# Kernel tuning notes

Measured on AMD Instinct MI355X. Metric: run time of the kernel, lower is better.

## Reference

```python
import jax, jax.numpy as jnp
import numpy as np


def setup_inputs() -> dict:
    key = jax.random.key(0)
    k1, k2, k3, k4 = jax.random.split(key, 4)
    B, S, D, H = 64, 512, 1024, 1024
    scale = 1.0 / np.sqrt(H)
    x = jax.random.normal(k1, (B, S, D), dtype=jnp.float32)
    Wx = jax.random.normal(k2, (D, H), dtype=jnp.float32) * scale
    Wh = jax.random.normal(k3, (H, H), dtype=jnp.float32) * scale
    b = jax.random.normal(k4, (H,), dtype=jnp.float32) * scale
    return {"x": x, "Wx": Wx, "Wh": Wh, "b": b}


def reference(x, Wx, Wh, b):
    # Elman tanh RNN cell: h_t = tanh(x_t @ Wx + h_{t-1} @ Wh + b)
    # Truncated BPTT: carried state is detached each step (stop_gradient),
    # matching `state = state.detach()` in the torch forward.
    B, S, D = x.shape
    H = Wh.shape[0]
    h0 = jnp.zeros((B, H), dtype=x.dtype)  # get_initial_state
    # precompute input projections for all timesteps: [S, B, H]
    xw = jnp.swapaxes(jnp.einsum('bsd,dh->bsh', x, Wx) + b, 0, 1)

    def step(h_prev, xw_t):
        h_new = jnp.tanh(xw_t + h_prev @ Wh)
        return jax.lax.stop_gradient(h_new), h_new

    _, hs = jax.lax.scan(step, h0, xw)  # hs: [S, B, H]
    return jnp.swapaxes(hs, 0, 1)  # [B, S, H]
```

## Files before the change

### kernel.cpp

```cpp
#include <hip/hip_runtime.h>
#include <stdint.h>

#define B_  64
#define S_  512
#define D_  1024
#define H_  1024

#define NBLK2 128

typedef __attribute__((ext_vector_type(2))) float    f32x2;
typedef __attribute__((ext_vector_type(4))) float    f32x4;
typedef __attribute__((ext_vector_type(4))) uint32_t u32x4;
typedef __attribute__((ext_vector_type(8))) __bf16   bf16x8;

__device__ __forceinline__ f32x4 mfma16(bf16x8 a, bf16x8 b, f32x4 c) {
  return __builtin_amdgcn_mfma_f32_16x16x32_bf16(a, b, c, 0, 0, 0);
}

__device__ __forceinline__ void gload_lds16(const void* g, void* l) {
  __builtin_amdgcn_global_load_lds(
      (const __attribute__((address_space(1))) void*)g,
      (__attribute__((address_space(3))) void*)l, 16, 0, 0);
}

__device__ __forceinline__ void st_dword_sc(uint32_t* p, uint32_t v) {
  asm volatile("global_store_dword %0, %1, off sc0 sc1" :: "v"(p), "v"(v) : "memory");
}
__device__ __forceinline__ void st_short_sc(uint16_t* p, uint32_t v) {
  asm volatile("global_store_short %0, %1, off sc0 sc1" :: "v"(p), "v"(v) : "memory");
}
__device__ __forceinline__ uint32_t ld_dword_sc(const uint32_t* p) {
  uint32_t r;
  asm volatile("global_load_dword %0, %1, off sc0 sc1\n\t"
               "s_waitcnt vmcnt(0)" : "=v"(r) : "v"(p) : "memory");
  return r;
}
__device__ __forceinline__ void ld_dwordx4_sc_issue(u32x4& dst, const void* p) {
  asm volatile("global_load_dwordx4 %0, %1, off sc0 sc1" : "=v"(dst) : "v"(p));
}

__device__ __forceinline__ uint32_t permhi(uint32_t a, uint32_t b) {
  return __builtin_amdgcn_perm(a, b, 0x07060302u);
}

__device__ __forceinline__ float tanh_fast(float x) {
  float ax = fabsf(x);
  float e = __expf(-2.0f * ax);
  float r = (1.0f - e) / (1.0f + e);
  return x < 0.0f ? -r : r;
}

__device__ __forceinline__ void split8(f32x4 a0, f32x4 a1, bf16x8& hi, bf16x8& lo) {
  float f[8] = {a0.x, a0.y, a0.z, a0.w, a1.x, a1.y, a1.z, a1.w};
  uint32_t hb[8], lb[8];
#pragma unroll
  for (int i = 0; i < 8; ++i) {
    uint32_t b = __builtin_bit_cast(uint32_t, f[i]);
    hb[i] = b;
    float hf = __builtin_bit_cast(float, b & 0xffff0000u);
    lb[i] = __builtin_bit_cast(uint32_t, f[i] - hf);
  }
  u32x4 hv = {permhi(hb[1], hb[0]), permhi(hb[3], hb[2]),
              permhi(hb[5], hb[4]), permhi(hb[7], hb[6])};
  u32x4 lv = {permhi(lb[1], lb[0]), permhi(lb[3], lb[2]),
              permhi(lb[5], lb[4]), permhi(lb[7], lb[6])};
  hi = __builtin_bit_cast(bf16x8, hv);
  lo = __builtin_bit_cast(bf16x8, lv);
}

__global__ __launch_bounds__(256) void prep_kernel(
    const float* __restrict__ Wx, const float* __restrict__ Wh,
    uint16_t* __restrict__ wxt_hi, uint16_t* __restrict__ wxt_lo,
    uint16_t* __restrict__ wht_hi, uint16_t* __restrict__ wht_lo,
    unsigned* __restrict__ flags)
{
  if (blockIdx.x == 0) {
    for (int i = threadIdx.x; i < 1024; i += 256)
      st_dword_sc((uint32_t*)flags + i, 0u);
  }
  __shared__ float tile[32][33];
  int bid = blockIdx.x;
  int mat = bid >> 10;
  int t   = bid & 1023;
  int tk = t >> 5, tn = t & 31;
  const float* src = mat ? Wh : Wx;
  uint16_t* dhi = mat ? wht_hi : wxt_hi;
  uint16_t* dlo = mat ? wht_lo : wxt_lo;
  int tx = threadIdx.x & 31, ty0 = threadIdx.x >> 5;
  int k0 = tk * 32, n0 = tn * 32;
#pragma unroll
  for (int i = 0; i < 4; ++i) {
    int ty = ty0 + 8 * i;
    tile[ty][tx] = src[(size_t)(k0 + ty) * 1024 + n0 + tx];
  }
  __syncthreads();
#pragma unroll
  for (int i = 0; i < 4; ++i) {
    int ty = ty0 + 8 * i;
    float v = tile[tx][ty];
    uint32_t bv = __builtin_bit_cast(uint32_t, v);
    float lo = v - __builtin_bit_cast(float, bv & 0xffff0000u);
    uint32_t lbv = __builtin_bit_cast(uint32_t, lo);
    size_t o = (size_t)(n0 + ty) * 1024 + k0 + tx;
    dhi[o] = (uint16_t)(bv >> 16);
    dlo[o] = (uint16_t)(lbv >> 16);
  }
}

__global__ __launch_bounds__(256) void xw_gemm_kernel(
    const float* __restrict__ x, const uint16_t* __restrict__ wxt_hi,
    const uint16_t* __restrict__ wxt_lo, const float* __restrict__ bias,
    float* __restrict__ out)
{
  __shared__ __align__(16) float    ldsA[128 * 32];
  __shared__ __align__(16) uint16_t ldsBh[128 * 32];
  __shared__ __align__(16) uint16_t ldsBl[128 * 32];

  int bid = blockIdx.x;
  int swz = (bid & 7) * 256 + (bid >> 3);
  int mt = swz >> 3, nt = swz & 7;
  int M0 = mt * 128, N0 = nt * 128;

  int tid = threadIdx.x;
  int w = tid >> 6, l = tid & 63;
  int wm = w >> 1, wn = w & 1;

  int a_row = l >> 3;
  int a_sw  = ((l & 7) ^ (l >> 3)) << 4;
  int b_row = l >> 2;
  int b_sw  = (((l & 3) ^ ((l >> 2) & 3)) << 4);

  f32x4 acc[4][4];
#pragma unroll
  for (int i = 0; i < 4; ++i)
#pragma unroll
    for (int j = 0; j < 4; ++j) acc[i][j] = (f32x4){0.f, 0.f, 0.f, 0.f};

  const char* xb  = (const char*)x;
  const char* bhp = (const char*)wxt_hi;
  const char* blp = (const char*)wxt_lo;

  for (int s = 0; s < 32; ++s) {
#pragma unroll
    for (int j = 0; j < 4; ++j) {
      int i = 4 * w + j;
      const char* g = xb + ((size_t)(M0 + 8 * i + a_row) * 4096) + s * 128 + a_sw;
      gload_lds16(g, (char*)ldsA + i * 1024);
    }
#pragma unroll
    for (int j = 0; j < 2; ++j) {
      int i = 2 * w + j;
      size_t ro = (size_t)(N0 + 16 * i + b_row) * 2048 + s * 64 + b_sw;
      gload_lds16(bhp + ro, (char*)ldsBh + i * 1024);
      gload_lds16(blp + ro, (char*)ldsBl + i * 1024);
    }
    __syncthreads();

    bf16x8 ah[4], al[4], bh[4], bl[4];
#pragma unroll
    for (int mi = 0; mi < 4; ++mi) {
      int row = 64 * wm + 16 * mi + (l & 15);
      int kb  = (l >> 4) * 32;
      int sw  = (row & 7) << 4;
      f32x4 a0 = *(const f32x4*)((const char*)ldsA + row * 128 + (kb ^ sw));
      f32x4 a1 = *(const f32x4*)((const char*)ldsA + row * 128 + ((kb + 16) ^ sw));
      split8(a0, a1, ah[mi], al[mi]);
    }
#pragma unroll
    for (int ni = 0; ni < 4; ++ni) {
      int n  = 64 * wn + 16 * ni + (l & 15);
      int kb = (l >> 4) * 16;
      int off = n * 64 + (kb ^ ((n & 3) << 4));
      bh[ni] = *(const bf16x8*)((const char*)ldsBh + off);
      bl[ni] = *(const bf16x8*)((const char*)ldsBl + off);
    }
#pragma unroll
    for (int mi = 0; mi < 4; ++mi)
#pragma unroll
      for (int ni = 0; ni < 4; ++ni) {
        acc[mi][ni] = mfma16(ah[mi], bh[ni], acc[mi][ni]);
        acc[mi][ni] = mfma16(al[mi], bh[ni], acc[mi][ni]);
        acc[mi][ni] = mfma16(ah[mi], bl[ni], acc[mi][ni]);
      }
    __syncthreads();
  }

#pragma unroll
  for (int ni = 0; ni < 4; ++ni) {
    int col = N0 + 64 * wn + 16 * ni + (l & 15);
    float bv = bias[col];
#pragma unroll
    for (int mi = 0; mi < 4; ++mi) {
      int row0 = M0 + 64 * wm + 16 * mi + 4 * (l >> 4);
#pragma unroll
      for (int r = 0; r < 4; ++r)
        out[(size_t)(row0 + r) * 1024 + col] = acc[mi][ni][r] + bv;
    }
  }
}

__global__ __launch_bounds__(512, 1) void rnn_seq_kernel(
    float* __restrict__ out,
    const uint16_t* wht_hi, const uint16_t* wht_lo,
    uint16_t* __restrict__ hq,
    unsigned* __restrict__ flags)
{
  __shared__ __align__(16) float red[2][8][16][33];

  const int bid = blockIdx.x;
  const int g   = bid >> 5;
  const int c   = bid & 31;
  const int c0  = c * 32;

  const int tid = threadIdx.x;
  const int kw  = tid >> 6;
  const int l   = tid & 63;
  const int lr  = l & 15, lq = l >> 4;

  u32x4 wbh[2][4], wbl[2][4];
#pragma unroll
  for (int n2 = 0; n2 < 2; ++n2) {
    const size_t colb = (size_t)(c0 + n2 * 16 + lr) * 1024 + kw * 128 + lq * 8;
#pragma unroll
    for (int kc = 0; kc < 4; ++kc) {
      wbh[n2][kc] = *(const u32x4*)(wht_hi + colb + kc * 32);
      wbl[n2][kc] = *(const u32x4*)(wht_lo + colb + kc * 32);
    }
  }

  const uint16_t* hb_base = hq + (size_t)(g * 16 + lr) * 1024 + kw * 128 + lq * 8;
  const int HQ = 64 * 1024;

  const int frow = tid >> 5;
  const int fcol = tid & 31;
  const size_t out_base = ((size_t)(g * 16 + frow) * 512) * 1024 + c0 + fcol;
  const size_t h_off    = (size_t)(g * 16 + frow) * 1024 + c0 + fcol;

  const uint32_t* fpoll = (const uint32_t*)flags + g * 256 + kw * 32 + (l & 31);
  uint32_t*       fown  = (uint32_t*)flags + g * 256 + c * 8 + kw;

  for (int t = 0; t < 512; ++t) {
#pragma unroll
    for (int n2 = 0; n2 < 2; ++n2)
#pragma unroll
      for (int kc = 0; kc < 4; ++kc) {
        asm volatile("" : "+v"(wbh[n2][kc]));
        asm volatile("" : "+v"(wbl[n2][kc]));
      }

    float xwv = out[out_base + (size_t)t * 1024];

    f32x4 cH0 = {0.f,0.f,0.f,0.f}, cL0 = {0.f,0.f,0.f,0.f};
    f32x4 cH1 = {0.f,0.f,0.f,0.f}, cL1 = {0.f,0.f,0.f,0.f};

    if (t > 0) {
      const unsigned tgt = (unsigned)t;
      while (true) {
        unsigned v = ld_dword_sc(fpoll);
        if (!__any((int)(v < tgt))) break;
        __builtin_amdgcn_s_sleep(1);
      }
      const uint16_t* hb = hb_base + ((t - 1) & 1) * HQ;
      u32x4 av[4];
#pragma unroll
      for (int kc = 0; kc < 4; ++kc)
        ld_dwordx4_sc_issue(av[kc], hb + kc * 32);
      __builtin_amdgcn_sched_barrier(0);
      asm volatile("s_waitcnt vmcnt(0)" ::: "memory");
      __builtin_amdgcn_sched_barrier(0);
#pragma unroll
      for (int kc = 0; kc < 4; ++kc) {
        bf16x8 a   = __builtin_bit_cast(bf16x8, av[kc]);
        cH0 = mfma16(a, __builtin_bit_cast(bf16x8, wbh[0][kc]), cH0);
        cH1 = mfma16(a, __builtin_bit_cast(bf16x8, wbh[1][kc]), cH1);
        cL0 = mfma16(a, __builtin_bit_cast(bf16x8, wbl[0][kc]), cL0);
        cL1 = mfma16(a, __builtin_bit_cast(bf16x8, wbl[1][kc]), cL1);
      }
    }

    f32x4 acc0 = cH0 + cL0;
    f32x4 acc1 = cH1 + cL1;

    const int rbuf = t & 1;
#pragma unroll
    for (int r = 0; r < 4; ++r) {
      red[rbuf][kw][lq * 4 + r][lr]      = acc0[r];
      red[rbuf][kw][lq * 4 + r][16 + lr] = acc1[r];
    }
    __syncthreads();

    float s = 0.f;
#pragma unroll
    for (int wv = 0; wv < 8; ++wv)
      s += red[rbuf][wv][frow][fcol];

    float hval = tanh_fast(s + xwv);
    out[out_base + (size_t)t * 1024] = hval;

    if (t < 511) {
      uint32_t b  = __builtin_bit_cast(uint32_t, hval);
      uint32_t rb = (b + 0x7fffu + ((b >> 16) & 1u)) >> 16;
      st_short_sc(hq + (size_t)(t & 1) * HQ + h_off, rb);
      asm volatile("s_waitcnt vmcnt(0)" ::: "memory");
      if (l == 0) st_dword_sc(fown, (uint32_t)(t + 1));
    }
  }
}

extern "C" void kernel_launch(void* const* d_in, const int* in_sizes, int n_in,
                              void* d_out, int out_size, void* d_ws, size_t ws_size,
                              hipStream_t stream) {
  const float* x    = (const float*)d_in[0];
  const float* Wx   = (const float*)d_in[1];
  const float* Wh   = (const float*)d_in[2];
  const float* bias = (const float*)d_in[3];
  float* out = (float*)d_out;

  char* ws = (char*)d_ws;
  uint16_t* wxt_hi = (uint16_t*)(ws);
  uint16_t* wxt_lo = (uint16_t*)(ws + (2u << 20));
  uint16_t* wht_hi = (uint16_t*)(ws + (4u << 20));
  uint16_t* wht_lo = (uint16_t*)(ws + (6u << 20));
  uint16_t* hq     = (uint16_t*)(ws + (8u << 20));
  unsigned* flags  = (unsigned*)(ws + (8u << 20) + (1u << 18));

  prep_kernel<<<dim3(2048), dim3(256), 0, stream>>>(Wx, Wh, wxt_hi, wxt_lo,
                                                    wht_hi, wht_lo, flags);
  xw_gemm_kernel<<<dim3(2048), dim3(256), 0, stream>>>(x, wxt_hi, wxt_lo, bias, out);
  rnn_seq_kernel<<<dim3(NBLK2), dim3(512), 0, stream>>>(out, wht_hi, wht_lo,
                                                        hq, flags);
}
```

Baseline: 1.730 ms.

## Replace flag polling with step-tagged hidden-state words for inter-block sync

```diff
diff --git a/kernel.cpp b/kernel.cpp
--- a/kernel.cpp
+++ b/kernel.cpp
@@ -25,15 +25,6 @@
 
 __device__ __forceinline__ void st_dword_sc(uint32_t* p, uint32_t v) {
   asm volatile("global_store_dword %0, %1, off sc0 sc1" :: "v"(p), "v"(v) : "memory");
-}
-__device__ __forceinline__ void st_short_sc(uint16_t* p, uint32_t v) {
-  asm volatile("global_store_short %0, %1, off sc0 sc1" :: "v"(p), "v"(v) : "memory");
-}
-__device__ __forceinline__ uint32_t ld_dword_sc(const uint32_t* p) {
-  uint32_t r;
-  asm volatile("global_load_dword %0, %1, off sc0 sc1\n\t"
-               "s_waitcnt vmcnt(0)" : "=v"(r) : "v"(p) : "memory");
-  return r;
 }
 __device__ __forceinline__ void ld_dwordx4_sc_issue(u32x4& dst, const void* p) {
   asm volatile("global_load_dwordx4 %0, %1, off sc0 sc1" : "=v"(dst) : "v"(p));
@@ -72,11 +63,11 @@
     const float* __restrict__ Wx, const float* __restrict__ Wh,
     uint16_t* __restrict__ wxt_hi, uint16_t* __restrict__ wxt_lo,
     uint16_t* __restrict__ wht_hi, uint16_t* __restrict__ wht_lo,
-    unsigned* __restrict__ flags)
+    uint32_t* __restrict__ hq)
 {
-  if (blockIdx.x == 0) {
-    for (int i = threadIdx.x; i < 1024; i += 256)
-      st_dword_sc((uint32_t*)flags + i, 0u);
+  {
+    int gid = blockIdx.x * 256 + threadIdx.x;
+    if (gid < 2 * 64 * 1024) hq[gid] = 0xFFFFFFFFu;
   }
   __shared__ float tile[32][33];
   int bid = blockIdx.x;
@@ -202,8 +193,7 @@
 __global__ __launch_bounds__(512, 1) void rnn_seq_kernel(
     float* __restrict__ out,
     const uint16_t* wht_hi, const uint16_t* wht_lo,
-    uint16_t* __restrict__ hq,
-    unsigned* __restrict__ flags)
+    uint32_t* __restrict__ hq)
 {
   __shared__ __align__(16) float red[2][8][16][33];
 
@@ -228,7 +218,7 @@
     }
   }
 
-  const uint16_t* hb_base = hq + (size_t)(g * 16 + lr) * 1024 + kw * 128 + lq * 8;
+  const uint32_t* hq_base = hq + (size_t)(g * 16 + lr) * 1024 + kw * 128 + lq * 8;
   const int HQ = 64 * 1024;
 
   const int frow = tid >> 5;
@@ -236,9 +226,6 @@
   const size_t out_base = ((size_t)(g * 16 + frow) * 512) * 1024 + c0 + fcol;
   const size_t h_off    = (size_t)(g * 16 + frow) * 1024 + c0 + fcol;
 
-  const uint32_t* fpoll = (const uint32_t*)flags + g * 256 + kw * 32 + (l & 31);
-  uint32_t*       fown  = (uint32_t*)flags + g * 256 + c * 8 + kw;
-
   for (int t = 0; t < 512; ++t) {
 #pragma unroll
     for (int n2 = 0; n2 < 2; ++n2)
@@ -254,23 +241,38 @@
     f32x4 cH1 = {0.f,0.f,0.f,0.f}, cL1 = {0.f,0.f,0.f,0.f};
 
     if (t > 0) {
-      const unsigned tgt = (unsigned)t;
+      const uint32_t* hb = hq_base + ((t - 1) & 1) * HQ;
+      const uint32_t expect = (uint32_t)(t - 1) & 0xffffu;
+      u32x4 pk[4][2];
       while (true) {
-        unsigned v = ld_dword_sc(fpoll);
-        if (!__any((int)(v < tgt))) break;
+#pragma unroll
+        for (int kc = 0; kc < 4; ++kc) {
+          ld_dwordx4_sc_issue(pk[kc][0], hb + kc * 32);
+          ld_dwordx4_sc_issue(pk[kc][1], hb + kc * 32 + 4);
+        }
+        __builtin_amdgcn_sched_barrier(0);
+        asm volatile("s_waitcnt vmcnt(0)" ::: "memory");
+        __builtin_amdgcn_sched_barrier(0);
+        uint32_t bad = 0;
+#pragma unroll
+        for (int kc = 0; kc < 4; ++kc)
+#pragma unroll
+          for (int j = 0; j < 2; ++j)
+#pragma unroll
+            for (int e = 0; e < 4; ++e)
+              bad |= (pk[kc][j][e] ^ expect);
+        bad &= 0xffffu;
+        if (!__any((int)bad)) break;
         __builtin_amdgcn_s_sleep(1);
       }
-      const uint16_t* hb = hb_base + ((t - 1) & 1) * HQ;
-      u32x4 av[4];
-#pragma unroll
-      for (int kc = 0; kc < 4; ++kc)
-        ld_dwordx4_sc_issue(av[kc], hb + kc * 32);
-      __builtin_amdgcn_sched_barrier(0);
-      asm volatile("s_waitcnt vmcnt(0)" ::: "memory");
-      __builtin_amdgcn_sched_barrier(0);
 #pragma unroll
       for (int kc = 0; kc < 4; ++kc) {
-        bf16x8 a   = __builtin_bit_cast(bf16x8, av[kc]);
+        u32x4 aw;
+        aw[0] = permhi(pk[kc][0][1], pk[kc][0][0]);
+        aw[1] = permhi(pk[kc][0][3], pk[kc][0][2]);
+        aw[2] = permhi(pk[kc][1][1], pk[kc][1][0]);
+        aw[3] = permhi(pk[kc][1][3], pk[kc][1][2]);
+        bf16x8 a = __builtin_bit_cast(bf16x8, aw);
         cH0 = mfma16(a, __builtin_bit_cast(bf16x8, wbh[0][kc]), cH0);
         cH1 = mfma16(a, __builtin_bit_cast(bf16x8, wbh[1][kc]), cH1);
         cL0 = mfma16(a, __builtin_bit_cast(bf16x8, wbl[0][kc]), cL0);
@@ -295,15 +297,13 @@
       s += red[rbuf][wv][frow][fcol];
 
     float hval = tanh_fast(s + xwv);
-    out[out_base + (size_t)t * 1024] = hval;
 
     if (t < 511) {
       uint32_t b  = __builtin_bit_cast(uint32_t, hval);
-      uint32_t rb = (b + 0x7fffu + ((b >> 16) & 1u)) >> 16;
-      st_short_sc(hq + (size_t)(t & 1) * HQ + h_off, rb);
-      asm volatile("s_waitcnt vmcnt(0)" ::: "memory");
-      if (l == 0) st_dword_sc(fown, (uint32_t)(t + 1));
-    }
+      uint32_t hi = (b + 0x7fffu + ((b >> 16) & 1u)) & 0xffff0000u;
+      st_dword_sc(hq + (size_t)(t & 1) * HQ + h_off, hi | (uint32_t)t);
+    }
+    out[out_base + (size_t)t * 1024] = hval;
   }
 }
 
@@ -321,12 +321,10 @@
   uint16_t* wxt_lo = (uint16_t*)(ws + (2u << 20));
   uint16_t* wht_hi = (uint16_t*)(ws + (4u << 20));
   uint16_t* wht_lo = (uint16_t*)(ws + (6u << 20));
-  uint16_t* hq     = (uint16_t*)(ws + (8u << 20));
-  unsigned* flags  = (unsigned*)(ws + (8u << 20) + (1u << 18));
+  uint32_t* hq     = (uint32_t*)(ws + (8u << 20));
 
   prep_kernel<<<dim3(2048), dim3(256), 0, stream>>>(Wx, Wh, wxt_hi, wxt_lo,
-                                                    wht_hi, wht_lo, flags);
+                                                    wht_hi, wht_lo, hq);
   xw_gemm_kernel<<<dim3(2048), dim3(256), 0, stream>>>(x, wxt_hi, wxt_lo, bias, out);
-  rnn_seq_kernel<<<dim3(NBLK2), dim3(512), 0, stream>>>(out, wht_hi, wht_lo,
-                                                        hq, flags);
-}
+  rnn_seq_kernel<<<dim3(NBLK2), dim3(512), 0, stream>>>(out, wht_hi, wht_lo, hq);
+}
```

New measurement: 1.751 ms. No clear change (+1.2%).
